# Optimization experiments

Measured on AMD Instinct MI355X. Metric: run time of the kernel, lower is better.

## Reference

```python
import jax, jax.numpy as jnp
import numpy as np

D = 256
H = 8
DK = D // H
FF = 4 * D
EPS = 1e-5


def layer_norm(x, g, b):
    mu = jnp.mean(x, axis=-1, keepdims=True)
    var = jnp.mean(jnp.square(x - mu), axis=-1, keepdims=True)
    return (x - mu) * jax.lax.rsqrt(var + EPS) * g + b


def setup_inputs() -> dict:
    key = jax.random.key(0)
    ks = jax.random.split(key, 12)
    s = 0.02
    return {
        "x": jax.random.normal(ks[0], (4, 2048, D), jnp.float32),
        "Wq": jax.random.normal(ks[1], (D, D), jnp.float32) * s,
        "Wk": jax.random.normal(ks[2], (D, D), jnp.float32) * s,
        "Wv": jax.random.normal(ks[3], (D, D), jnp.float32) * s,
        "Wo": jax.random.normal(ks[4], (D, D), jnp.float32) * s,
        "W1": jax.random.normal(ks[5], (D, FF), jnp.float32) * s,
        "W2": jax.random.normal(ks[6], (D, FF), jnp.float32) * s,
        "Wout": jax.random.normal(ks[7], (FF, D), jnp.float32) * s,
        "g1": jnp.ones((D,), jnp.float32),
        "b1": jnp.zeros((D,), jnp.float32),
        "g2": jnp.ones((D,), jnp.float32),
        "b2": jnp.zeros((D,), jnp.float32),
    }


def reference(x, Wq, Wk, Wv, Wo, W1, W2, Wout, g1, b1, g2, b2):
    B, S, _ = x.shape
    # --- multi-head attention (manual matmul + softmax + matmul) ---
    q = (x @ Wq).reshape(B, S, H, DK).transpose(0, 2, 1, 3)  # [B,H,S,DK]
    k = (x @ Wk).reshape(B, S, H, DK).transpose(0, 2, 1, 3)
    v = (x @ Wv).reshape(B, S, H, DK).transpose(0, 2, 1, 3)
    scores = jnp.einsum("bhqd,bhkd->bhqk", q, k) * (DK ** -0.5)  # [B,H,S,S]
    probs = jax.nn.softmax(scores, axis=-1)
    o = jnp.einsum("bhqk,bhkd->bhqd", probs, v)
    attn = o.transpose(0, 2, 1, 3).reshape(B, S, D) @ Wo
    # --- GLU feedforward with dual LayerNorms ---
    x1 = layer_norm(x + attn, g1, b1)
    xw = jax.nn.silu(x1 @ W1)
    xv = x1 @ W2
    out = (xw * xv) @ Wout
    return layer_norm(x1 + out, g2, b2)
```

## Files before the change

kernel.cpp:

```cpp
#include <hip/hip_runtime.h>

#define D 256
#define H 8
#define DK 32
#define FF 1024
#define SEQ 2048
#define BATCH 4
#define MROWS (BATCH * SEQ)
#define LN_EPS 1e-5f
#define QSCALE (0.1767766952966369f * 1.4426950408889634f)
#define LOG2E 1.4426950408889634f

typedef unsigned short u16;
typedef unsigned int u32;
typedef __attribute__((ext_vector_type(8))) short bf16x8;
typedef __attribute__((ext_vector_type(4))) float f32x4;

#define MFMA16(a, b, c) __builtin_amdgcn_mfma_f32_16x16x32_bf16(a, b, c, 0, 0, 0)

#if __has_builtin(__builtin_amdgcn_exp2f)
#define EXP2(x) __builtin_amdgcn_exp2f(x)
#else
#define EXP2(x) exp2f(x)
#endif
#if __has_builtin(__builtin_amdgcn_rcpf)
#define RCPF(x) __builtin_amdgcn_rcpf(x)
#else
#define RCPF(x) (1.f / (x))
#endif

__device__ __forceinline__ u16 f2bf(float f) {
    union { float f; u32 u; } x; x.f = f;
    u32 r = x.u + 0x7fffu + ((x.u >> 16) & 1u);
    return (u16)(r >> 16);
}
__device__ __forceinline__ u32 pack2(float a, float b) {
    return (u32)f2bf(a) | ((u32)f2bf(b) << 16);
}
__device__ __forceinline__ u32 pktrunc(float a, float b) {
    u32 ua = __builtin_bit_cast(u32, a), ub = __builtin_bit_cast(u32, b);
    return __builtin_amdgcn_perm(ub, ua, 0x07060302u);
}
__device__ __forceinline__ float silu_f(float x) {
    return x * RCPF(1.f + EXP2(-x * LOG2E));
}

__global__ void stage_w(const float* __restrict__ Wq, const float* __restrict__ Wk,
                        const float* __restrict__ Wv, const float* __restrict__ Wo,
                        const float* __restrict__ W1, const float* __restrict__ W2,
                        const float* __restrict__ Wout, u16* __restrict__ dst) {
    __shared__ float T[64][65];
    int bid = blockIdx.x, tid = threadIdx.x;
    const float* src;
    size_t dbase;
    int K, N, tile;
    float sc = 1.f;
    if (bid < 64) {
        int which = bid >> 4;
        tile = bid & 15;
        src = which == 0 ? Wq : which == 1 ? Wk : which == 2 ? Wv : Wo;
        if (which == 0) sc = QSCALE;
        dbase = (size_t)which << 16;
        K = 256; N = 256;
    } else if (bid < 192) {
        int which = (bid - 64) >> 6;
        tile = (bid - 64) & 63;
        src = which ? W2 : W1;
        dbase = 262144 + (size_t)which * 262144;
        K = 256; N = 1024;
    } else {
        tile = bid - 192;
        src = Wout;
        dbase = 786432;
        K = 1024; N = 256;
    }
    int ntn = N >> 6;
    int k0 = (tile / ntn) << 6, n0 = (tile % ntn) << 6;
#pragma unroll
    for (int p = 0; p < 4; p++) {
        int r = p * 16 + (tid >> 4), c = (tid & 15) * 4;
        float4 v = *(const float4*)(src + (size_t)(k0 + r) * N + n0 + c);
        T[c + 0][r] = v.x * sc;
        T[c + 1][r] = v.y * sc;
        T[c + 2][r] = v.z * sc;
        T[c + 3][r] = v.w * sc;
    }
    __syncthreads();
#pragma unroll
    for (int p = 0; p < 4; p++) {
        int n = p * 16 + (tid >> 4), k = (tid & 15) * 4;
        uint2 o;
        o.x = pack2(T[n][k], T[n][k + 1]);
        o.y = pack2(T[n][k + 2], T[n][k + 3]);
        *(uint2*)(dst + dbase + (size_t)(n0 + n) * K + k0 + k) = o;
    }
}

__global__ void gemm_qkv(const float* __restrict__ X, const u16* __restrict__ Bt,
                         u16* __restrict__ Qo, u16* __restrict__ Ko,
                         u16* __restrict__ Vo) {
    int gid = (blockIdx.x * 256 + threadIdx.x) >> 6;
    int lane = threadIdx.x & 63;
    int mt = gid / 12, ng = gid - mt * 12;
    int m0 = mt << 5, n0 = ng << 6;
    int m = lane & 15, quad = lane >> 4;
    const float* xp0 = X + (size_t)(m0 + m) * D + quad * 8;
    const float* xp1 = xp0 + (size_t)16 * D;
    const u16* bp = Bt + (size_t)(n0 + m) * D + quad * 8;
    f32x4 acc[2][4] = {{{0,0,0,0},{0,0,0,0},{0,0,0,0},{0,0,0,0}},
                       {{0,0,0,0},{0,0,0,0},{0,0,0,0},{0,0,0,0}}};
    for (int k0 = 0; k0 < D; k0 += 32) {
        float4 f0 = *(const float4*)(xp0 + k0);
        float4 f1 = *(const float4*)(xp0 + k0 + 4);
        float4 f2 = *(const float4*)(xp1 + k0);
        float4 f3 = *(const float4*)(xp1 + k0 + 4);
        uint4 u0, u1;
        u0.x = pktrunc(f0.x, f0.y); u0.y = pktrunc(f0.z, f0.w);
        u0.z = pktrunc(f1.x, f1.y); u0.w = pktrunc(f1.z, f1.w);
        u1.x = pktrunc(f2.x, f2.y); u1.y = pktrunc(f2.z, f2.w);
        u1.z = pktrunc(f3.x, f3.y); u1.w = pktrunc(f3.z, f3.w);
        bf16x8 a0 = __builtin_bit_cast(bf16x8, u0);
        bf16x8 a1 = __builtin_bit_cast(bf16x8, u1);
#pragma unroll
        for (int t = 0; t < 4; t++) {
            bf16x8 bv = *(const bf16x8*)(bp + (size_t)t * 16 * D + k0);
            acc[0][t] = MFMA16(a0, bv, acc[0][t]);
            acc[1][t] = MFMA16(a1, bv, acc[1][t]);
        }
    }
    int seg = n0 >> 8;
    int nc0 = n0 & 255;
    if (seg < 2) {
        u16* out = seg ? Ko : Qo;
#pragma unroll
        for (int u = 0; u < 2; u++) {
            int row = m0 + u * 16 + (quad << 2);
#pragma unroll
            for (int t = 0; t < 4; t++) {
                int col = nc0 + t * 16 + m;
#pragma unroll
                for (int r = 0; r < 4; r++)
                    out[(size_t)(row + r) * D + col] = f2bf(acc[u][t][r]);
            }
        }
    } else {
#pragma unroll
        for (int u = 0; u < 2; u++) {
            int row = m0 + u * 16 + (quad << 2);
            int b = row >> 11, sl = row & 2047;
#pragma unroll
            for (int t = 0; t < 4; t++) {
                int col = nc0 + t * 16 + m;
                int hh = col >> 5, dk = col & 31;
                size_t base = ((size_t)(b * 8 + hh) * 32 + dk) * SEQ + sl;
                uint2 pk;
                pk.x = pack2(acc[u][t][0], acc[u][t][1]);
                pk.y = pack2(acc[u][t][2], acc[u][t][3]);
                *(uint2*)(Vo + base) = pk;
            }
        }
    }
}

__global__ __launch_bounds__(256, 8)
void attn_mfma(const u16* __restrict__ Q, const u16* __restrict__ Km,
               const u16* __restrict__ Vt, u16* __restrict__ O) {
    __shared__ __align__(16) u16 Kt[2][64][36];
    __shared__ __align__(16) u16 Vl[2][32][68];
    int tid = threadIdx.x;
    int lane = tid & 63;
    int m = lane & 15, quad = lane >> 4;
    int w = tid >> 6;
    int bid = blockIdx.x;
    int qb = bid & 63;
    int bh = bid >> 6;
    int b = bh >> 3, h = bh & 7;
    int q0 = qb * 32 + (w & 1) * 16;
    int hb = w >> 1;
    size_t rowbase = (size_t)b * SEQ;

    bf16x8 qa = *(const bf16x8*)(Q + (rowbase + q0 + m) * D + h * DK + quad * 8);

    const u16* kg = Km + rowbase * D + h * DK;
    const u16* vg = Vt + (size_t)bh * DK * SEQ;

    int krow = tid >> 2, kseg = tid & 3;
    int skv = (krow & 32) | (((krow >> 2) & 3) << 3) | (((krow >> 4) & 1) << 2) | (krow & 3);
    int vrow = tid >> 3, vseg = tid & 7;

    uint4 kreg = *(const uint4*)(kg + (size_t)skv * D + kseg * 8);
    uint4 vreg = *(const uint4*)(vg + (size_t)vrow * SEQ + vseg * 8);
    *(uint4*)(&Kt[0][krow][kseg * 8]) = kreg;
    *(uint4*)(&Vl[0][vrow][vseg * 8]) = vreg;

    f32x4 o0 = {0,0,0,0}, o1 = {0,0,0,0};
    float ls = 0.f;

    for (int i = 0; i < SEQ / 64; i++) {
        int buf = i & 1;
        if (i + 1 < SEQ / 64) {
            int kvn = (i + 1) * 64;
            kreg = *(const uint4*)(kg + (size_t)(kvn + skv) * D + kseg * 8);
            vreg = *(const uint4*)(vg + (size_t)vrow * SEQ + kvn + vseg * 8);
        }
        __syncthreads();
        f32x4 z = {0,0,0,0};
        f32x4 s0, s1;
        {
            bf16x8 kb0 = *(const bf16x8*)(&Kt[buf][(2 * hb) * 16 + m][quad * 8]);
            bf16x8 kb1 = *(const bf16x8*)(&Kt[buf][(2 * hb + 1) * 16 + m][quad * 8]);
            s0 = MFMA16(kb0, qa, z);
            s1 = MFMA16(kb1, qa, z);
        }
        {
            float pa0 = EXP2(s0[0]), pa1 = EXP2(s0[1]);
            float pa2 = EXP2(s0[2]), pa3 = EXP2(s0[3]);
            float pb0 = EXP2(s1[0]), pb1 = EXP2(s1[1]);
            float pb2 = EXP2(s1[2]), pb3 = EXP2(s1[3]);
            ls += ((pa0 + pa1) + (pa2 + pa3)) + ((pb0 + pb1) + (pb2 + pb3));
            uint4 pw;
            pw.x = pktrunc(pa0, pa1);
            pw.y = pktrunc(pa2, pa3);
            pw.z = pktrunc(pb0, pb1);
            pw.w = pktrunc(pb2, pb3);
            bf16x8 pfrag = __builtin_bit_cast(bf16x8, pw);
            bf16x8 vb0 = *(const bf16x8*)(&Vl[buf][m][hb * 32 + quad * 8]);
            bf16x8 vb1 = *(const bf16x8*)(&Vl[buf][16 + m][hb * 32 + quad * 8]);
            o0 = MFMA16(pfrag, vb0, o0);
            o1 = MFMA16(pfrag, vb1, o1);
        }
        if (i + 1 < SEQ / 64) {
            *(uint4*)(&Kt[buf ^ 1][krow][kseg * 8]) = kreg;
            *(uint4*)(&Vl[buf ^ 1][vrow][vseg * 8]) = vreg;
        }
    }
    ls += __shfl_xor(ls, 16);
    ls += __shfl_xor(ls, 32);
    __syncthreads();
    float* comb = (float*)&Kt[0][0][0];
    if (w >= 2) {
        float* c = comb + ((size_t)(w - 2) * 64 + lane) * 9;
#pragma unroll
        for (int r = 0; r < 4; r++) { c[r] = o0[r]; c[4 + r] = o1[r]; }
        c[8] = ls;
    }
    __syncthreads();
    if (w < 2) {
        const float* c = comb + ((size_t)w * 64 + lane) * 9;
#pragma unroll
        for (int r = 0; r < 4; r++) { o0[r] += c[r]; o1[r] += c[4 + r]; }
        ls += c[8];
        u16* ob = O + (rowbase + q0 + quad * 4) * D + h * DK;
#pragma unroll
        for (int r = 0; r < 4; r++) {
            float lr = __shfl(ls, quad * 4 + r);
            float inv = 1.f / lr;
            ob[(size_t)r * D + m] = f2bf(o0[r] * inv);
            ob[(size_t)r * D + 16 + m] = f2bf(o1[r] * inv);
        }
    }
}

__global__ __launch_bounds__(256, 2)
void wo_res_ln(const u16* __restrict__ A, const u16* __restrict__ Bt,
               const float* __restrict__ res, const float* __restrict__ g,
               const float* __restrict__ bb, float* __restrict__ outf,
               u16* __restrict__ outb) {
    __shared__ float Sy[4][16], Sq[4][16], Mu[16], Rs[16];
    int tid = threadIdx.x;
    int w = tid >> 6, lane = tid & 63;
    int m = lane & 15, quad = lane >> 4;
    int m0 = blockIdx.x << 4, n0 = w << 6;
    const u16* ap = A + (size_t)(m0 + m) * D + quad * 8;
    const u16* bp = Bt + (size_t)(n0 + m) * D + quad * 8;
    f32x4 acc[4] = {{0,0,0,0},{0,0,0,0},{0,0,0,0},{0,0,0,0}};
#pragma unroll
    for (int k0 = 0; k0 < D; k0 += 32) {
        bf16x8 a0 = *(const bf16x8*)(ap + k0);
#pragma unroll
        for (int t = 0; t < 4; t++)
            acc[t] = MFMA16(a0, *(const bf16x8*)(bp + (size_t)t * 16 * D + k0), acc[t]);
    }
#pragma unroll
    for (int r = 0; r < 4; r++) {
        int row = (quad << 2) + r;
        float sy = 0.f, sq = 0.f;
#pragma unroll
        for (int t = 0; t < 4; t++) {
            float y = acc[t][r] + res[(size_t)(m0 + row) * D + n0 + t * 16 + m];
            acc[t][r] = y;
            sy += y;
            sq += y * y;
        }
        sy += __shfl_xor(sy, 1); sq += __shfl_xor(sq, 1);
        sy += __shfl_xor(sy, 2); sq += __shfl_xor(sq, 2);
        sy += __shfl_xor(sy, 4); sq += __shfl_xor(sq, 4);
        sy += __shfl_xor(sy, 8); sq += __shfl_xor(sq, 8);
        if (m == 0) { Sy[w][row] = sy; Sq[w][row] = sq; }
    }
    __syncthreads();
    if (tid < 16) {
        float s = Sy[0][tid] + Sy[1][tid] + Sy[2][tid] + Sy[3][tid];
        float q = Sq[0][tid] + Sq[1][tid] + Sq[2][tid] + Sq[3][tid];
        float mu = s * (1.f / 256.f);
        float var = q * (1.f / 256.f) - mu * mu;
        Mu[tid] = mu;
        Rs[tid] = rsqrtf(var + LN_EPS);
    }
    __syncthreads();
#pragma unroll
    for (int r = 0; r < 4; r++) {
        int row = (quad << 2) + r;
        float mu = Mu[row], rs = Rs[row];
#pragma unroll
        for (int t = 0; t < 4; t++) {
            int col = n0 + t * 16 + m;
            float yv = (acc[t][r] - mu) * rs * g[col] + bb[col];
            outf[(size_t)(m0 + row) * D + col] = yv;
            outb[(size_t)(m0 + row) * D + col] = f2bf(yv);
        }
    }
}

__global__ __launch_bounds__(512, 2)
void glu_ws(const u16* __restrict__ x1b, const u16* __restrict__ W1t,
            const u16* __restrict__ W2t, u16* __restrict__ G) {
    __shared__ __align__(16) u16 WL[2][64][260];
    int tid = threadIdx.x;
    int w = tid >> 6, lane = tid & 63;
    int m = lane & 15, quad = lane >> 4;
    int cg = blockIdx.x & 15, rg = blockIdx.x >> 4;
    int n0 = cg << 6;
#pragma unroll
    for (int i = 0; i < 4; i++) {
        int idx = i * 512 + tid;
        int row = idx >> 5, seg = idx & 31;
        *(uint4*)(&WL[0][row][seg * 8]) =
            *(const uint4*)(W1t + (size_t)(n0 + row) * D + seg * 8);
        *(uint4*)(&WL[1][row][seg * 8]) =
            *(const uint4*)(W2t + (size_t)(n0 + row) * D + seg * 8);
    }
    __syncthreads();
    int mr = rg * 512 + w * 64;
    f32x4 a1[4][4], a2[4][4];
#pragma unroll
    for (int u = 0; u < 4; u++)
#pragma unroll
        for (int t = 0; t < 4; t++) {
            a1[u][t] = (f32x4){0.f, 0.f, 0.f, 0.f};
            a2[u][t] = (f32x4){0.f, 0.f, 0.f, 0.f};
        }
#pragma unroll
    for (int k0 = 0; k0 < D; k0 += 32) {
        bf16x8 av[4];
#pragma unroll
        for (int u = 0; u < 4; u++)
            av[u] = *(const bf16x8*)(x1b + (size_t)(mr + u * 16 + m) * D + k0 + quad * 8);
#pragma unroll
        for (int t = 0; t < 4; t++) {
            bf16x8 w1 = *(const bf16x8*)(&WL[0][t * 16 + m][k0 + quad * 8]);
            bf16x8 w2 = *(const bf16x8*)(&WL[1][t * 16 + m][k0 + quad * 8]);
#pragma unroll
            for (int u = 0; u < 4; u++) {
                a1[u][t] = MFMA16(av[u], w1, a1[u][t]);
                a2[u][t] = MFMA16(av[u], w2, a2[u][t]);
            }
        }
    }
#pragma unroll
    for (int u = 0; u < 4; u++) {
        int row = mr + u * 16 + (quad << 2);
#pragma unroll
        for (int t = 0; t < 4; t++) {
            int col = n0 + t * 16 + m;
#pragma unroll
            for (int r = 0; r < 4; r++)
                G[(size_t)(row + r) * FF + col] = f2bf(silu_f(a1[u][t][r]) * a2[u][t][r]);
        }
    }
}

__global__ __launch_bounds__(1024, 4)
void wout_ln(const u16* __restrict__ G, const u16* __restrict__ Woutt,
             const float* __restrict__ x1f, const float* __restrict__ g,
             const float* __restrict__ bb, float* __restrict__ outf) {
    __shared__ __align__(16) u16 Gl[32][1044];
    __shared__ float Sy[16][32], Sq[16][32], Mu[32], Rs[32];
    int tid = threadIdx.x;
    int w = tid >> 6, lane = tid & 63;
    int m = lane & 15, quad = lane >> 4;
    int m0 = blockIdx.x << 5;
#pragma unroll
    for (int i = 0; i < 4; i++) {
        int idx = i * 1024 + tid;
        int row = idx >> 7, seg = idx & 127;
        *(uint4*)(&Gl[row][seg * 8]) =
            *(const uint4*)(G + (size_t)(m0 + row) * FF + seg * 8);
    }
    __syncthreads();
    int n0p = w << 4;
    const u16* bp = Woutt + (size_t)(n0p + m) * FF + quad * 8;
    f32x4 acc[2] = {{0,0,0,0},{0,0,0,0}};
#pragma unroll 4
    for (int k0 = 0; k0 < FF; k0 += 32) {
        bf16x8 a0 = *(const bf16x8*)(&Gl[m][k0 + quad * 8]);
        bf16x8 a1v = *(const bf16x8*)(&Gl[16 + m][k0 + quad * 8]);
        bf16x8 bv = *(const bf16x8*)(bp + k0);
        acc[0] = MFMA16(a0, bv, acc[0]);
        acc[1] = MFMA16(a1v, bv, acc[1]);
    }
#pragma unroll
    for (int u = 0; u < 2; u++) {
#pragma unroll
        for (int r = 0; r < 4; r++) {
            int row = u * 16 + (quad << 2) + r;
            float y = acc[u][r] + x1f[(size_t)(m0 + row) * D + n0p + m];
            acc[u][r] = y;
            float sy = y, sq = y * y;
            sy += __shfl_xor(sy, 1); sq += __shfl_xor(sq, 1);
            sy += __shfl_xor(sy, 2); sq += __shfl_xor(sq, 2);
            sy += __shfl_xor(sy, 4); sq += __shfl_xor(sq, 4);
            sy += __shfl_xor(sy, 8); sq += __shfl_xor(sq, 8);
            if (m == 0) { Sy[w][row] = sy; Sq[w][row] = sq; }
        }
    }
    __syncthreads();
    if (tid < 32) {
        float s = 0.f, q = 0.f;
#pragma unroll
        for (int ww = 0; ww < 16; ww++) { s += Sy[ww][tid]; q += Sq[ww][tid]; }
        float mu = s * (1.f / 256.f);
        float var = q * (1.f / 256.f) - mu * mu;
        Mu[tid] = mu;
        Rs[tid] = rsqrtf(var + LN_EPS);
    }
    __syncthreads();
#pragma unroll
    for (int u = 0; u < 2; u++) {
#pragma unroll
        for (int r = 0; r < 4; r++) {
            int row = u * 16 + (quad << 2) + r;
            int col = n0p + m;
            outf[(size_t)(m0 + row) * D + col] =
                (acc[u][r] - Mu[row]) * Rs[row] * g[col] + bb[col];
        }
    }
}

#define WS_WQKVT  ((size_t)0)
#define WS_WOT    ((size_t)196608)
#define WS_W1T    ((size_t)262144)
#define WS_W2T    ((size_t)524288)
#define WS_WOUTT  ((size_t)786432)
#define WS_Q      ((size_t)1048576)
#define WS_K      ((size_t)3145728)
#define WS_VT     ((size_t)5242880)
#define WS_O      ((size_t)7340032)
#define WS_GATED  ((size_t)1048576)
#define WS_X1F    ((size_t)9437184)
#define WS_X1B    ((size_t)13631488)

extern "C" void kernel_launch(void* const* d_in, const int* in_sizes, int n_in,
                              void* d_out, int out_size, void* d_ws, size_t ws_size,
                              hipStream_t stream) {
    const float* x    = (const float*)d_in[0];
    const float* Wq   = (const float*)d_in[1];
    const float* Wk   = (const float*)d_in[2];
    const float* Wv   = (const float*)d_in[3];
    const float* Wo   = (const float*)d_in[4];
    const float* W1   = (const float*)d_in[5];
    const float* W2   = (const float*)d_in[6];
    const float* Wout = (const float*)d_in[7];
    const float* g1   = (const float*)d_in[8];
    const float* b1   = (const float*)d_in[9];
    const float* g2   = (const float*)d_in[10];
    const float* b2   = (const float*)d_in[11];

    u16* ws = (u16*)d_ws;
    float* x1f = (float*)(ws + WS_X1F);

    stage_w<<<256, 256, 0, stream>>>(Wq, Wk, Wv, Wo, W1, W2, Wout, ws + WS_WQKVT);

    gemm_qkv<<<768, 256, 0, stream>>>(x, ws + WS_WQKVT,
                                      ws + WS_Q, ws + WS_K, ws + WS_VT);

    attn_mfma<<<2048, 256, 0, stream>>>(ws + WS_Q, ws + WS_K, ws + WS_VT, ws + WS_O);

    wo_res_ln<<<512, 256, 0, stream>>>(ws + WS_O, ws + WS_WOT, x, g1, b1,
                                       x1f, ws + WS_X1B);

    glu_ws<<<256, 512, 0, stream>>>(ws + WS_X1B, ws + WS_W1T, ws + WS_W2T,
                                    ws + WS_GATED);

    wout_ln<<<256, 1024, 0, stream>>>(ws + WS_GATED, ws + WS_WOUTT, x1f,
                                      g2, b2, (float*)d_out);
}
```

Measured before the change: 195.0 us.

## Stage QKV weight tile in LDS and share it across eight waves

Measured after the change: 184.0 us. -5.6%, faster.

```diff
diff --git a/kernel.cpp b/kernel.cpp
--- a/kernel.cpp
+++ b/kernel.cpp
@@ -96,68 +96,64 @@
     }
 }
 
-__global__ void gemm_qkv(const float* __restrict__ X, const u16* __restrict__ Bt,
-                         u16* __restrict__ Qo, u16* __restrict__ Ko,
-                         u16* __restrict__ Vo) {
-    int gid = (blockIdx.x * 256 + threadIdx.x) >> 6;
-    int lane = threadIdx.x & 63;
-    int mt = gid / 12, ng = gid - mt * 12;
-    int m0 = mt << 5, n0 = ng << 6;
+__global__ __launch_bounds__(512, 3)
+void gemm_qkv(const float* __restrict__ X, const u16* __restrict__ Bt,
+              u16* __restrict__ Qo, u16* __restrict__ Ko,
+              u16* __restrict__ Vo) {
+    __shared__ __align__(16) u16 WL[64][260];
+    int tid = threadIdx.x;
+    int w = tid >> 6, lane = tid & 63;
     int m = lane & 15, quad = lane >> 4;
-    const float* xp0 = X + (size_t)(m0 + m) * D + quad * 8;
-    const float* xp1 = xp0 + (size_t)16 * D;
-    const u16* bp = Bt + (size_t)(n0 + m) * D + quad * 8;
-    f32x4 acc[2][4] = {{{0,0,0,0},{0,0,0,0},{0,0,0,0},{0,0,0,0}},
-                       {{0,0,0,0},{0,0,0,0},{0,0,0,0},{0,0,0,0}}};
+    int cg = blockIdx.x % 12, rg = blockIdx.x / 12;
+    int n0 = cg << 6;
+#pragma unroll
+    for (int i = 0; i < 4; i++) {
+        int idx = i * 512 + tid;
+        int row = idx >> 5, seg = idx & 31;
+        *(uint4*)(&WL[row][seg * 8]) =
+            *(const uint4*)(Bt + (size_t)(n0 + row) * D + seg * 8);
+    }
+    __syncthreads();
+    int m0 = rg * 128 + w * 16;
+    const float* xp = X + (size_t)(m0 + m) * D + quad * 8;
+    f32x4 acc[4] = {{0,0,0,0},{0,0,0,0},{0,0,0,0},{0,0,0,0}};
+#pragma unroll
     for (int k0 = 0; k0 < D; k0 += 32) {
-        float4 f0 = *(const float4*)(xp0 + k0);
-        float4 f1 = *(const float4*)(xp0 + k0 + 4);
-        float4 f2 = *(const float4*)(xp1 + k0);
-        float4 f3 = *(const float4*)(xp1 + k0 + 4);
-        uint4 u0, u1;
+        float4 f0 = *(const float4*)(xp + k0);
+        float4 f1 = *(const float4*)(xp + k0 + 4);
+        uint4 u0;
         u0.x = pktrunc(f0.x, f0.y); u0.y = pktrunc(f0.z, f0.w);
         u0.z = pktrunc(f1.x, f1.y); u0.w = pktrunc(f1.z, f1.w);
-        u1.x = pktrunc(f2.x, f2.y); u1.y = pktrunc(f2.z, f2.w);
-        u1.z = pktrunc(f3.x, f3.y); u1.w = pktrunc(f3.z, f3.w);
         bf16x8 a0 = __builtin_bit_cast(bf16x8, u0);
-        bf16x8 a1 = __builtin_bit_cast(bf16x8, u1);
-#pragma unroll
-        for (int t = 0; t < 4; t++) {
-            bf16x8 bv = *(const bf16x8*)(bp + (size_t)t * 16 * D + k0);
-            acc[0][t] = MFMA16(a0, bv, acc[0][t]);
-            acc[1][t] = MFMA16(a1, bv, acc[1][t]);
-        }
-    }
-    int seg = n0 >> 8;
-    int nc0 = n0 & 255;
+#pragma unroll
+        for (int t = 0; t < 4; t++) {
+            bf16x8 bv = *(const bf16x8*)(&WL[t * 16 + m][k0 + quad * 8]);
+            acc[t] = MFMA16(a0, bv, acc[t]);
+        }
+    }
+    int seg = cg >> 2;
+    int nc0 = (cg & 3) << 6;
+    int row = m0 + (quad << 2);
     if (seg < 2) {
         u16* out = seg ? Ko : Qo;
 #pragma unroll
-        for (int u = 0; u < 2; u++) {
-            int row = m0 + u * 16 + (quad << 2);
-#pragma unroll
-            for (int t = 0; t < 4; t++) {
-                int col = nc0 + t * 16 + m;
-#pragma unroll
-                for (int r = 0; r < 4; r++)
-                    out[(size_t)(row + r) * D + col] = f2bf(acc[u][t][r]);
-            }
+        for (int t = 0; t < 4; t++) {
+            int col = nc0 + t * 16 + m;
+#pragma unroll
+            for (int r = 0; r < 4; r++)
+                out[(size_t)(row + r) * D + col] = f2bf(acc[t][r]);
         }
     } else {
-#pragma unroll
-        for (int u = 0; u < 2; u++) {
-            int row = m0 + u * 16 + (quad << 2);
-            int b = row >> 11, sl = row & 2047;
-#pragma unroll
-            for (int t = 0; t < 4; t++) {
-                int col = nc0 + t * 16 + m;
-                int hh = col >> 5, dk = col & 31;
-                size_t base = ((size_t)(b * 8 + hh) * 32 + dk) * SEQ + sl;
-                uint2 pk;
-                pk.x = pack2(acc[u][t][0], acc[u][t][1]);
-                pk.y = pack2(acc[u][t][2], acc[u][t][3]);
-                *(uint2*)(Vo + base) = pk;
-            }
+        int b = row >> 11, sl = row & 2047;
+#pragma unroll
+        for (int t = 0; t < 4; t++) {
+            int col = nc0 + t * 16 + m;
+            int hh = col >> 5, dk = col & 31;
+            size_t base = ((size_t)(b * 8 + hh) * 32 + dk) * SEQ + sl;
+            uint2 pk;
+            pk.x = pack2(acc[t][0], acc[t][1]);
+            pk.y = pack2(acc[t][2], acc[t][3]);
+            *(uint2*)(Vo + base) = pk;
         }
     }
 }
@@ -481,7 +477,7 @@
 
     stage_w<<<256, 256, 0, stream>>>(Wq, Wk, Wv, Wo, W1, W2, Wout, ws + WS_WQKVT);
 
-    gemm_qkv<<<768, 256, 0, stream>>>(x, ws + WS_WQKVT,
+    gemm_qkv<<<768, 512, 0, stream>>>(x, ws + WS_WQKVT,
                                       ws + WS_Q, ws + WS_K, ws + WS_VT);
 
     attn_mfma<<<2048, 256, 0, stream>>>(ws + WS_Q, ws + WS_K, ws + WS_VT, ws + WS_O);
```
